# Optimization experiments

Hardware: AMD Instinct MI355X
Metric: run time of the kernel (lower is better)

The kernel has to match this reference:

```python
import jax, jax.numpy as jnp
import numpy as np

N_NODES = 50000
N_GRAPHS = 512
HIDDEN = 128
BN_EPS = 1e-5


def setup_inputs() -> dict:
    key = jax.random.key(0)
    ks = jax.random.split(key, 16)
    E = 800000
    x = jax.random.normal(ks[0], (N_NODES, 1), dtype=jnp.float32)
    pos = jax.random.normal(ks[1], (N_NODES, 3), dtype=jnp.float32)
    edge_index = jax.random.randint(ks[2], (2, E), 0, N_NODES, dtype=jnp.int64)
    batch = jnp.sort(jax.random.randint(ks[3], (N_NODES,), 0, N_GRAPHS, dtype=jnp.int64))

    def lin(k, fan_in, fan_out):
        bound = 1.0 / np.sqrt(fan_in)
        return jax.random.uniform(k, (fan_in, fan_out), jnp.float32, -bound, bound)

    # conv1: in=1 -> concat dim 2*1+3=5
    c1_w1 = lin(ks[4], 5, HIDDEN); c1_b1 = jnp.zeros((HIDDEN,), jnp.float32)
    c1_w2 = lin(ks[5], HIDDEN, HIDDEN); c1_b2 = jnp.zeros((HIDDEN,), jnp.float32)
    # conv2: in=128 -> concat dim 2*128+3=259
    c2_w1 = lin(ks[6], 2 * HIDDEN + 3, HIDDEN); c2_b1 = jnp.zeros((HIDDEN,), jnp.float32)
    c2_w2 = lin(ks[7], HIDDEN, HIDDEN); c2_b2 = jnp.zeros((HIDDEN,), jnp.float32)
    # predictor MLP [128, 128, 1], bias=[False, True], batch_norm + relu between
    p_w1 = lin(ks[8], HIDDEN, HIDDEN)
    bn_gamma = jnp.ones((HIDDEN,), jnp.float32)
    bn_beta = jnp.zeros((HIDDEN,), jnp.float32)
    p_w2 = lin(ks[9], HIDDEN, 1)
    p_b2 = jnp.zeros((1,), jnp.float32)
    return {
        "x": x, "pos": pos, "edge_index": edge_index, "batch": batch,
        "c1_w1": c1_w1, "c1_b1": c1_b1, "c1_w2": c1_w2, "c1_b2": c1_b2,
        "c2_w1": c2_w1, "c2_b1": c2_b1, "c2_w2": c2_w2, "c2_b2": c2_b2,
        "p_w1": p_w1, "bn_gamma": bn_gamma, "bn_beta": bn_beta,
        "p_w2": p_w2, "p_b2": p_b2,
    }


def _conv(x, pos, src, dst, w1, b1, w2, b2):
    # gather endpoints; PyG: x_j = x[src], x_i = x[dst], aggregate into dst
    feat = jnp.concatenate([x[dst], x[src], pos[src] - pos[dst]], axis=-1)  # [E, 2F+3]
    msg = jax.nn.relu(feat @ w1 + b1) @ w2 + b2  # [E, H]
    return jax.ops.segment_sum(msg, dst, num_segments=N_NODES)  # [N, H]


def reference(x, pos, edge_index, batch,
              c1_w1, c1_b1, c1_w2, c1_b2,
              c2_w1, c2_b1, c2_w2, c2_b2,
              p_w1, bn_gamma, bn_beta, p_w2, p_b2):
    src, dst = edge_index[0], edge_index[1]
    h = jax.nn.relu(_conv(x, pos, src, dst, c1_w1, c1_b1, c1_w2, c1_b2))
    h = jax.nn.relu(_conv(h, pos, src, dst, c2_w1, c2_b1, c2_w2, c2_b2))
    g = jax.ops.segment_sum(h, batch, num_segments=N_GRAPHS)  # [G, H] global add pool
    # predictor: Linear(no bias) -> BatchNorm(train stats) -> ReLU -> Linear(bias)
    z = g @ p_w1
    mean = jnp.mean(z, axis=0)
    var = jnp.var(z, axis=0)
    z = bn_gamma * (z - mean) * jax.lax.rsqrt(var + BN_EPS) + bn_beta
    z = jax.nn.relu(z)
    return z @ p_w2 + p_b2  # [G, 1]
```

## Files before the change

### kernel.cpp

```cpp
#include <hip/hip_runtime.h>
#include <hip/hip_bf16.h>

#define HID 128
#define DMAX 64
#define ESHARD 2048

typedef unsigned int uint;
typedef unsigned short ushort;
using short8 = __attribute__((ext_vector_type(8))) short;
using f32x4  = __attribute__((ext_vector_type(4))) float;

#define MFMA_B16(a, b, c) __builtin_amdgcn_mfma_f32_16x16x32_bf16(a, b, c, 0, 0, 0)

__device__ inline ushort bf16rn(float f) {
  uint u = __float_as_uint(f);
  u += 0x7fff + ((u >> 16) & 1);
  return (ushort)(u >> 16);
}
__device__ inline uint packbf(float a, float b) {
  return (uint)bf16rn(a) | ((uint)bf16rn(b) << 16);
}
__device__ inline float bflo(uint u) { return __uint_as_float(u << 16); }
__device__ inline float bfhi(uint u) { return __uint_as_float(u & 0xffff0000u); }

__global__ __launch_bounds__(256) void k_prep(
    const float* __restrict__ x, const float* __restrict__ pos,
    const float* __restrict__ c1w2, const float* __restrict__ c2w1, const float* __restrict__ c2w2,
    float4* __restrict__ xp, int* __restrict__ deg, float* __restrict__ g,
    float* __restrict__ mv,
    ushort* __restrict__ w1t, ushort* __restrict__ wdt,
    ushort* __restrict__ wst, ushort* __restrict__ w2t,
    int N, int G, int Npad) {
  int idx = blockIdx.x * 256 + threadIdx.x;
  if (idx < Npad) deg[idx] = 0;
  if (idx < G * HID) g[idx] = 0.f;
  if (idx < 256) mv[idx] = 0.f;
  if (idx < N) {
    xp[idx] = make_float4(pos[3 * idx], pos[3 * idx + 1], pos[3 * idx + 2], x[idx]);
  }
  {
    int m = idx >> 14, e = idx & 16383;
    int c = e >> 7, k = e & 127;
    const float* src;
    ushort* dst;
    if (m == 0)      { src = c1w2;              dst = w1t; }
    else if (m == 1) { src = c2w1;              dst = wdt; }
    else if (m == 2) { src = c2w1 + 128 * 128;  dst = wst; }
    else             { src = c2w2;              dst = w2t; }
    dst[e] = bf16rn(src[k * 128 + c]);
  }
}

__global__ __launch_bounds__(256) void k_build(const int* __restrict__ dstv,
                                               const int* __restrict__ srcv,
                                               int* __restrict__ deg, int* __restrict__ srcsP,
                                               int E) {
  int shard = blockIdx.x & 7;
  int base = (blockIdx.x >> 3) * ESHARD;
  int lim = min(base + ESHARD, E);
  for (int e = base + threadIdx.x; e < lim; e += 256) {
    int d = dstv[e];
    if (((d >> 5) & 7) == shard) {
      int s = srcv[e];
      int r = atomicAdd(&deg[d], 1);
      if (r < DMAX) srcsP[(size_t)d * DMAX + r] = s;
    }
  }
}

__global__ __launch_bounds__(64) void k_conv1(
    const float4* __restrict__ xp,
    const int* __restrict__ deg, const int* __restrict__ srcsP,
    const float* __restrict__ w1, const float* __restrict__ b1, uint* __restrict__ hs) {
  int n = blockIdx.x;
  int lane = threadIdx.x;
  int f0 = 2 * lane;
  __shared__ float sxs[64];
  __shared__ float sdp[3][64];
  int cnt = min(deg[n], DMAX);
  float4 me = xp[n];
  float xi = me.w;
  float2 a1 = *(const float2*)&w1[HID + f0];
  float2 a2 = *(const float2*)&w1[2 * HID + f0];
  float2 a3 = *(const float2*)&w1[3 * HID + f0];
  float2 a4 = *(const float2*)&w1[4 * HID + f0];
  float c_0 = fmaf(xi, w1[f0],     b1[f0]);
  float c_1 = fmaf(xi, w1[f0 + 1], b1[f0 + 1]);
  float acc0 = 0.f, acc1 = 0.f;
  if (lane < cnt) {
    int s = srcsP[(size_t)n * DMAX + lane];
    float4 v = xp[s];
    sxs[lane] = v.w;
    sdp[0][lane] = v.x - me.x;
    sdp[1][lane] = v.y - me.y;
    sdp[2][lane] = v.z - me.z;
  }
  __syncthreads();
  for (int k = 0; k < cnt; ++k) {
    float xj = sxs[k], d0 = sdp[0][k], d1 = sdp[1][k], d2 = sdp[2][k];
    float h0 = fmaf(xj, a1.x, fmaf(d0, a2.x, fmaf(d1, a3.x, fmaf(d2, a4.x, c_0))));
    float h1 = fmaf(xj, a1.y, fmaf(d0, a2.y, fmaf(d1, a3.y, fmaf(d2, a4.y, c_1))));
    acc0 += fmaxf(h0, 0.f);
    acc1 += fmaxf(h1, 0.f);
  }
  hs[(size_t)n * 64 + lane] = packbf(acc0, acc1);
}

__global__ __launch_bounds__(512) void k_mfuse(
    const ushort* __restrict__ A, const ushort* __restrict__ W1t,
    const ushort* __restrict__ Wdt, const ushort* __restrict__ Wst,
    const float* __restrict__ b1, const float* __restrict__ bd,
    const int* __restrict__ deg,
    uint* __restrict__ psb, uint* __restrict__ pdb, int M) {
  __shared__ uint hl[128][68];
  __shared__ uint hd[128][68];
  int t = threadIdx.x;
  int l = t & 63;
  int rl = l & 15, kg = l >> 4;
  int wv = t >> 6;
  int rs = wv >> 2;
  int ct = wv & 3;
  int rowbase = blockIdx.x * 128 + rs * 64;
  short8 af[4][4];
  float dgv[4];
  #pragma unroll
  for (int rg = 0; rg < 4; ++rg) {
    int r = rowbase + rg * 16 + rl;
    int rc = min(r, M - 1);
    const short8* arow = (const short8*)(A + (size_t)rc * 128);
    #pragma unroll
    for (int k = 0; k < 4; ++k) af[rg][k] = arow[4 * k + kg];
    dgv[rg] = (r < M) ? (float)deg[r] : 0.f;
  }
  #pragma unroll
  for (int j = 0; j < 2; ++j) {
    int nt = ct * 2 + j;
    const short8* wrow = (const short8*)(W1t + (size_t)(nt * 16 + rl) * 128);
    short8 wf[4];
    #pragma unroll
    for (int k = 0; k < 4; ++k) wf[k] = wrow[4 * k + kg];
    int c0 = nt * 16 + kg * 4;
    f32x4 b4 = *(const f32x4*)&b1[c0];
    #pragma unroll
    for (int rg = 0; rg < 4; ++rg) {
      f32x4 acc = {0.f, 0.f, 0.f, 0.f};
      acc = MFMA_B16(wf[0], af[rg][0], acc);
      acc = MFMA_B16(wf[1], af[rg][1], acc);
      acc = MFMA_B16(wf[2], af[rg][2], acc);
      acc = MFMA_B16(wf[3], af[rg][3], acc);
      int rloc = rs * 64 + rg * 16 + rl;
      float v0 = fmaxf(fmaf(dgv[rg], b4[0], acc[0]), 0.f);
      float v1 = fmaxf(fmaf(dgv[rg], b4[1], acc[1]), 0.f);
      float v2 = fmaxf(fmaf(dgv[rg], b4[2], acc[2]), 0.f);
      float v3 = fmaxf(fmaf(dgv[rg], b4[3], acc[3]), 0.f);
      hl[rloc][(c0 >> 1)]     = packbf(v0, v1);
      hl[rloc][(c0 >> 1) + 1] = packbf(v2, v3);
    }
  }
  __syncthreads();
  #pragma unroll
  for (int rg = 0; rg < 4; ++rg) {
    const uint* hrow = hl[rs * 64 + rg * 16 + rl];
    #pragma unroll
    for (int k = 0; k < 4; ++k) af[rg][k] = *(const short8*)&hrow[k * 16 + kg * 4];
  }
  __syncthreads();
  bool isD = (ct >> 1) != 0;
  int ntb = (ct & 1) * 4;
  const ushort* Wm = isD ? Wdt : Wst;
  #pragma unroll
  for (int jj = 0; jj < 4; ++jj) {
    int nt = ntb + jj;
    const short8* wrow = (const short8*)(Wm + (size_t)(nt * 16 + rl) * 128);
    short8 wf[4];
    #pragma unroll
    for (int k = 0; k < 4; ++k) wf[k] = wrow[4 * k + kg];
    int c0 = nt * 16 + kg * 4;
    f32x4 b4 = {0.f, 0.f, 0.f, 0.f};
    if (isD) b4 = *(const f32x4*)&bd[c0];
    #pragma unroll
    for (int rg = 0; rg < 4; ++rg) {
      f32x4 acc = {0.f, 0.f, 0.f, 0.f};
      acc = MFMA_B16(wf[0], af[rg][0], acc);
      acc = MFMA_B16(wf[1], af[rg][1], acc);
      acc = MFMA_B16(wf[2], af[rg][2], acc);
      acc = MFMA_B16(wf[3], af[rg][3], acc);
      int rloc = rs * 64 + rg * 16 + rl;
      uint lo = packbf(acc[0] + b4[0], acc[1] + b4[1]);
      uint hi = packbf(acc[2] + b4[2], acc[3] + b4[3]);
      if (isD) {
        hd[rloc][(c0 >> 1)]     = lo;
        hd[rloc][(c0 >> 1) + 1] = hi;
      } else {
        hl[rloc][(c0 >> 1)]     = lo;
        hl[rloc][(c0 >> 1) + 1] = hi;
      }
    }
  }
  __syncthreads();
  int rb2 = blockIdx.x * 128;
  #pragma unroll
  for (int idx = t; idx < 128 * 16; idx += 512) {
    int row = idx >> 4, c4 = (idx & 15) * 4;
    int gr = rb2 + row;
    if (gr < M) {
      *(uint4*)&psb[(size_t)gr * 64 + c4] = *(const uint4*)&hl[row][c4];
      *(uint4*)&pdb[(size_t)gr * 64 + c4] = *(const uint4*)&hd[row][c4];
    }
  }
}

__global__ __launch_bounds__(64) void k_conv2(
    const float4* __restrict__ xp,
    const int* __restrict__ deg, const int* __restrict__ srcsP,
    const uint* __restrict__ pdb, const uint* __restrict__ ps,
    const float* __restrict__ wc, uint* __restrict__ hs) {
  int n = blockIdx.x;
  int lane = threadIdx.x;
  int eg = lane >> 4;
  int fb = lane & 15;
  int f0 = 8 * fb;
  __shared__ int ssrc[64];
  __shared__ float sdp[3][64];
  int cnt = min(deg[n], DMAX);
  float4 me = xp[n];
  float c0[8], c1[8], c2[8], pdv[8], acc[8];
  uint4 pdu = *(const uint4*)&pdb[(size_t)n * 64 + fb * 4];
  uint pdua[4] = {pdu.x, pdu.y, pdu.z, pdu.w};
  #pragma unroll
  for (int i = 0; i < 4; ++i) {
    pdv[2 * i]     = bflo(pdua[i]);
    pdv[2 * i + 1] = bfhi(pdua[i]);
  }
  #pragma unroll
  for (int i = 0; i < 8; ++i) {
    c0[i]  = wc[f0 + i];
    c1[i]  = wc[HID + f0 + i];
    c2[i]  = wc[2 * HID + f0 + i];
    acc[i] = 0.f;
  }
  if (lane < cnt) {
    int s = srcsP[(size_t)n * DMAX + lane];
    float4 v = xp[s];
    ssrc[lane] = s;
    sdp[0][lane] = v.x - me.x;
    sdp[1][lane] = v.y - me.y;
    sdp[2][lane] = v.z - me.z;
  }
  __syncthreads();
  for (int k = 0; k < cnt; k += 16) {
    int ke[4] = {k + eg, k + 4 + eg, k + 8 + eg, k + 12 + eg};
    int kc[4];
    #pragma unroll
    for (int j = 0; j < 4; ++j) kc[j] = min(ke[j], cnt - 1);
    int se[4] = {ssrc[kc[0]], ssrc[kc[1]], ssrc[kc[2]], ssrc[kc[3]]};
    uint4 u[4];
    #pragma unroll
    for (int j = 0; j < 4; ++j) u[j] = *(const uint4*)&ps[(size_t)se[j] * 64 + fb * 4];
    #pragma unroll
    for (int j = 0; j < 4; ++j) {
      float dd0 = sdp[0][kc[j]], dd1 = sdp[1][kc[j]], dd2 = sdp[2][kc[j]];
      bool vv = ke[j] < cnt;
      uint uu[4] = {u[j].x, u[j].y, u[j].z, u[j].w};
      if (vv) {
        #pragma unroll
        for (int q = 0; q < 4; ++q) {
          float w0  = pdv[2*q]   + fmaf(dd0, c0[2*q],   fmaf(dd1, c1[2*q],   dd2 * c2[2*q]));
          float w1v = pdv[2*q+1] + fmaf(dd0, c0[2*q+1], fmaf(dd1, c1[2*q+1], dd2 * c2[2*q+1]));
          acc[2*q]   += fmaxf(w0  + bflo(uu[q]), 0.f);
          acc[2*q+1] += fmaxf(w1v + bfhi(uu[q]), 0.f);
        }
      }
    }
  }
  #pragma unroll
  for (int i = 0; i < 8; ++i) {
    acc[i] += __shfl_xor(acc[i], 16);
    acc[i] += __shfl_xor(acc[i], 32);
  }
  if (eg == 0) {
    uint4 o;
    o.x = packbf(acc[0], acc[1]);
    o.y = packbf(acc[2], acc[3]);
    o.z = packbf(acc[4], acc[5]);
    o.w = packbf(acc[6], acc[7]);
    *(uint4*)&hs[(size_t)n * 64 + fb * 4] = o;
  }
}

__global__ __launch_bounds__(256) void k_mpool(
    const ushort* __restrict__ A, const ushort* __restrict__ Wt,
    const float* __restrict__ bias, const int* __restrict__ deg, const int* __restrict__ batch,
    float* __restrict__ Of, int M) {
  int t = threadIdx.x;
  int l = t & 63;
  int rl = l & 15, kg = l >> 4;
  int r = blockIdx.x * 64 + (t >> 6) * 16 + rl;
  int rc = min(r, M - 1);
  bool valid = (r < M);
  const short8* arow = (const short8*)(A + (size_t)rc * 128);
  short8 af0 = arow[kg], af1 = arow[4 + kg], af2 = arow[8 + kg], af3 = arow[12 + kg];
  float dg = valid ? (float)deg[r] : 0.f;
  int bt = batch[rc];
  int gf = __shfl(bt, 0);
  int gl = __shfl(bt, 15);
  #pragma unroll
  for (int nt = 0; nt < 8; ++nt) {
    const short8* wrow = (const short8*)(Wt + (size_t)(nt * 16 + rl) * 128);
    f32x4 acc = {0.f, 0.f, 0.f, 0.f};
    acc = MFMA_B16(wrow[kg],      af0, acc);
    acc = MFMA_B16(wrow[4 + kg],  af1, acc);
    acc = MFMA_B16(wrow[8 + kg],  af2, acc);
    acc = MFMA_B16(wrow[12 + kg], af3, acc);
    int c0 = nt * 16 + kg * 4;
    f32x4 b4 = *(const f32x4*)&bias[c0];
    float v0 = valid ? fmaxf(fmaf(dg, b4[0], acc[0]), 0.f) : 0.f;
    float v1 = valid ? fmaxf(fmaf(dg, b4[1], acc[1]), 0.f) : 0.f;
    float v2 = valid ? fmaxf(fmaf(dg, b4[2], acc[2]), 0.f) : 0.f;
    float v3 = valid ? fmaxf(fmaf(dg, b4[3], acc[3]), 0.f) : 0.f;
    for (int gg = gf; gg <= gl; ++gg) {
      bool mine = (bt == gg);
      float s0 = mine ? v0 : 0.f;
      float s1 = mine ? v1 : 0.f;
      float s2 = mine ? v2 : 0.f;
      float s3 = mine ? v3 : 0.f;
      #pragma unroll
      for (int m = 1; m <= 8; m <<= 1) {
        s0 += __shfl_xor(s0, m);
        s1 += __shfl_xor(s1, m);
        s2 += __shfl_xor(s2, m);
        s3 += __shfl_xor(s3, m);
      }
      if (rl == 0) {
        float* gp = &Of[(size_t)gg * 128 + c0];
        atomicAdd(gp + 0, s0);
        atomicAdd(gp + 1, s1);
        atomicAdd(gp + 2, s2);
        atomicAdd(gp + 3, s3);
      }
    }
  }
}

__global__ __launch_bounds__(256) void k_pgemm(
    const float* __restrict__ A, const float* __restrict__ W, float* __restrict__ O1,
    float* __restrict__ mv, int M) {
  __shared__ float As[128][36];
  int t = threadIdx.x;
  int n0 = blockIdx.x * 32;
  int j = t & 127, m = t >> 7;
  for (int idx = t; idx < 32 * 128; idx += 256) {
    int r = idx >> 7, i = idx & 127;
    int n = n0 + r;
    As[i][r] = (n < M) ? A[(size_t)n * 128 + i] : 0.f;
  }
  __syncthreads();
  float acc[16];
  #pragma unroll
  for (int r = 0; r < 16; ++r) acc[r] = 0.f;
  int rb = m * 16;
  for (int i = 0; i < 128; ++i) {
    float w = W[i * 128 + j];
    const float4* ap = reinterpret_cast<const float4*>(&As[i][rb]);
    #pragma unroll
    for (int q = 0; q < 4; ++q) {
      float4 a = ap[q];
      acc[q * 4 + 0] = fmaf(a.x, w, acc[q * 4 + 0]);
      acc[q * 4 + 1] = fmaf(a.y, w, acc[q * 4 + 1]);
      acc[q * 4 + 2] = fmaf(a.z, w, acc[q * 4 + 2]);
      acc[q * 4 + 3] = fmaf(a.w, w, acc[q * 4 + 3]);
    }
  }
  float S = 0.f, Q = 0.f;
  #pragma unroll
  for (int r = 0; r < 16; ++r) {
    int n = n0 + rb + r;
    if (n < M) {
      O1[(size_t)n * 128 + j] = acc[r];
      S += acc[r];
      Q = fmaf(acc[r], acc[r], Q);
    }
  }
  atomicAdd(&mv[j], S);
  atomicAdd(&mv[128 + j], Q);
}

__global__ __launch_bounds__(256) void k_final(
    const float* __restrict__ z, const float* __restrict__ mv,
    const float* __restrict__ gamma, const float* __restrict__ beta,
    const float* __restrict__ w2, const float* __restrict__ b2,
    float* __restrict__ out, int G) {
  int wid = threadIdx.x >> 6, lane = threadIdx.x & 63;
  int r = blockIdx.x * 4 + wid;
  if (r >= G) return;
  float acc = 0.f;
  float invG = 1.f / (float)G;
  #pragma unroll
  for (int h = 0; h < 2; ++h) {
    int jj = lane + h * 64;
    float mean = mv[jj] * invG;
    float var = mv[128 + jj] * invG - mean * mean;
    float rstd = rsqrtf(var + 1e-5f);
    float v = z[(size_t)r * 128 + jj];
    float zn = fmaf((v - mean) * rstd, gamma[jj], beta[jj]);
    acc = fmaf(fmaxf(zn, 0.f), w2[jj], acc);
  }
  #pragma unroll
  for (int off = 32; off; off >>= 1) acc += __shfl_down(acc, off);
  if (lane == 0) out[r] = acc + b2[0];
}

extern "C" void kernel_launch(void* const* d_in, const int* in_sizes, int n_in,
                              void* d_out, int out_size, void* d_ws, size_t ws_size,
                              hipStream_t stream) {
  const float* x     = (const float*)d_in[0];
  const float* pos   = (const float*)d_in[1];
  const int*   eidx  = (const int*)d_in[2];
  const int*   batch = (const int*)d_in[3];
  const float* c1w1  = (const float*)d_in[4];
  const float* c1b1  = (const float*)d_in[5];
  const float* c1w2  = (const float*)d_in[6];
  const float* c1b2  = (const float*)d_in[7];
  const float* c2w1  = (const float*)d_in[8];
  const float* c2b1  = (const float*)d_in[9];
  const float* c2w2  = (const float*)d_in[10];
  const float* c2b2  = (const float*)d_in[11];
  const float* pw1   = (const float*)d_in[12];
  const float* gamma = (const float*)d_in[13];
  const float* beta  = (const float*)d_in[14];
  const float* pw2   = (const float*)d_in[15];
  const float* pb2   = (const float*)d_in[16];
  (void)n_in; (void)ws_size;

  const int N = in_sizes[0];
  const int E = in_sizes[2] / 2;
  const int G = out_size;
  const int* srcv = eidx;
  const int* dstv = eidx + E;

  char* w = (char*)d_ws;
  size_t o = 0;
  auto carve = [&](size_t bytes) { void* p = w + o; o = (o + bytes + 255) & ~(size_t)255; return p; };
  int Npad = ((N + 255) / 256) * 256;
  int* deg    = (int*)carve((size_t)Npad * 4);
  int* srcsP  = (int*)carve((size_t)N * DMAX * 4);
  float4* xp  = (float4*)carve((size_t)N * 16);
  uint*   hs1  = (uint*)carve((size_t)N * 64 * 4);
  uint*   pdb  = (uint*)carve((size_t)N * 64 * 4);
  uint*   psb  = (uint*)carve((size_t)N * 64 * 4);
  uint*   hs2  = (uint*)carve((size_t)N * 64 * 4);
  ushort* w1t  = (ushort*)carve(16384 * 2);
  ushort* wdt  = (ushort*)carve(16384 * 2);
  ushort* wst  = (ushort*)carve(16384 * 2);
  ushort* w2t  = (ushort*)carve(16384 * 2);
  float* g    = (float*)carve((size_t)G * HID * 4);
  float* z    = (float*)carve((size_t)G * HID * 4);
  float* mv   = (float*)carve(256 * 4);

  k_prep<<<256, 256, 0, stream>>>(x, pos, c1w2, c2w1, c2w2,
                                  xp, deg, g, mv, w1t, wdt, wst, w2t, N, G, Npad);
  int nwin = (E + ESHARD - 1) / ESHARD;
  k_build<<<nwin * 8, 256, 0, stream>>>(dstv, srcv, deg, srcsP, E);

  k_conv1<<<N, 64, 0, stream>>>(xp, deg, srcsP, c1w1, c1b1, hs1);
  int gb128 = (N + 127) / 128;
  k_mfuse<<<gb128, 512, 0, stream>>>((const ushort*)hs1, w1t, wdt, wst, c1b2, c2b1, deg,
                                     psb, pdb, N);
  k_conv2<<<N, 64, 0, stream>>>(xp, deg, srcsP, pdb, psb, c2w1 + 256 * HID, hs2);
  int gb = (N + 63) / 64;
  k_mpool<<<gb, 256, 0, stream>>>((const ushort*)hs2, w2t, c2b2, deg, batch, g, N);
  k_pgemm<<<(G + 31) / 32, 256, 0, stream>>>(g, pw1, z, mv, G);
  k_final<<<(G + 3) / 4, 256, 0, stream>>>(z, mv, gamma, beta, pw2, pb2, (float*)d_out, G);
}
```

Baseline: 166.8 us.

## Retile pooled-MLP kernel so each wave covers 64 rows and 32 columns

```diff
diff --git a/kernel.cpp b/kernel.cpp
--- a/kernel.cpp
+++ b/kernel.cpp
@@ -288,55 +288,75 @@
   }
 }
 
-__global__ __launch_bounds__(256) void k_mpool(
+__global__ __launch_bounds__(512) void k_mpool(
     const ushort* __restrict__ A, const ushort* __restrict__ Wt,
     const float* __restrict__ bias, const int* __restrict__ deg, const int* __restrict__ batch,
     float* __restrict__ Of, int M) {
   int t = threadIdx.x;
   int l = t & 63;
   int rl = l & 15, kg = l >> 4;
-  int r = blockIdx.x * 64 + (t >> 6) * 16 + rl;
-  int rc = min(r, M - 1);
-  bool valid = (r < M);
-  const short8* arow = (const short8*)(A + (size_t)rc * 128);
-  short8 af0 = arow[kg], af1 = arow[4 + kg], af2 = arow[8 + kg], af3 = arow[12 + kg];
-  float dg = valid ? (float)deg[r] : 0.f;
-  int bt = batch[rc];
-  int gf = __shfl(bt, 0);
-  int gl = __shfl(bt, 15);
-  #pragma unroll
-  for (int nt = 0; nt < 8; ++nt) {
+  int wv = t >> 6;
+  int rs = wv >> 2;
+  int ct = wv & 3;
+  int rowbase = blockIdx.x * 128 + rs * 64;
+  short8 af[4][4];
+  float dgv[4];
+  int btv[4], gfv[4], glv[4];
+  bool valv[4];
+  #pragma unroll
+  for (int rg = 0; rg < 4; ++rg) {
+    int r = rowbase + rg * 16 + rl;
+    int rc = min(r, M - 1);
+    const short8* arow = (const short8*)(A + (size_t)rc * 128);
+    #pragma unroll
+    for (int k = 0; k < 4; ++k) af[rg][k] = arow[4 * k + kg];
+    valv[rg] = (r < M);
+    dgv[rg] = valv[rg] ? (float)deg[r] : 0.f;
+    int bt = batch[rc];
+    btv[rg] = bt;
+    gfv[rg] = __shfl(bt, 0);
+    glv[rg] = __shfl(bt, 15);
+  }
+  #pragma unroll
+  for (int j = 0; j < 2; ++j) {
+    int nt = ct * 2 + j;
     const short8* wrow = (const short8*)(Wt + (size_t)(nt * 16 + rl) * 128);
-    f32x4 acc = {0.f, 0.f, 0.f, 0.f};
-    acc = MFMA_B16(wrow[kg],      af0, acc);
-    acc = MFMA_B16(wrow[4 + kg],  af1, acc);
-    acc = MFMA_B16(wrow[8 + kg],  af2, acc);
-    acc = MFMA_B16(wrow[12 + kg], af3, acc);
+    short8 wf[4];
+    #pragma unroll
+    for (int k = 0; k < 4; ++k) wf[k] = wrow[4 * k + kg];
     int c0 = nt * 16 + kg * 4;
     f32x4 b4 = *(const f32x4*)&bias[c0];
-    float v0 = valid ? fmaxf(fmaf(dg, b4[0], acc[0]), 0.f) : 0.f;
-    float v1 = valid ? fmaxf(fmaf(dg, b4[1], acc[1]), 0.f) : 0.f;
-    float v2 = valid ? fmaxf(fmaf(dg, b4[2], acc[2]), 0.f) : 0.f;
-    float v3 = valid ? fmaxf(fmaf(dg, b4[3], acc[3]), 0.f) : 0.f;
-    for (int gg = gf; gg <= gl; ++gg) {
-      bool mine = (bt == gg);
-      float s0 = mine ? v0 : 0.f;
-      float s1 = mine ? v1 : 0.f;
-      float s2 = mine ? v2 : 0.f;
-      float s3 = mine ? v3 : 0.f;
-      #pragma unroll
-      for (int m = 1; m <= 8; m <<= 1) {
-        s0 += __shfl_xor(s0, m);
-        s1 += __shfl_xor(s1, m);
-        s2 += __shfl_xor(s2, m);
-        s3 += __shfl_xor(s3, m);
-      }
-      if (rl == 0) {
-        float* gp = &Of[(size_t)gg * 128 + c0];
-        atomicAdd(gp + 0, s0);
-        atomicAdd(gp + 1, s1);
-        atomicAdd(gp + 2, s2);
-        atomicAdd(gp + 3, s3);
+    #pragma unroll
+    for (int rg = 0; rg < 4; ++rg) {
+      f32x4 acc = {0.f, 0.f, 0.f, 0.f};
+      acc = MFMA_B16(wf[0], af[rg][0], acc);
+      acc = MFMA_B16(wf[1], af[rg][1], acc);
+      acc = MFMA_B16(wf[2], af[rg][2], acc);
+      acc = MFMA_B16(wf[3], af[rg][3], acc);
+      float v0 = valv[rg] ? fmaxf(fmaf(dgv[rg], b4[0], acc[0]), 0.f) : 0.f;
+      float v1 = valv[rg] ? fmaxf(fmaf(dgv[rg], b4[1], acc[1]), 0.f) : 0.f;
+      float v2 = valv[rg] ? fmaxf(fmaf(dgv[rg], b4[2], acc[2]), 0.f) : 0.f;
+      float v3 = valv[rg] ? fmaxf(fmaf(dgv[rg], b4[3], acc[3]), 0.f) : 0.f;
+      for (int gg = gfv[rg]; gg <= glv[rg]; ++gg) {
+        bool mine = (btv[rg] == gg);
+        float s0 = mine ? v0 : 0.f;
+        float s1 = mine ? v1 : 0.f;
+        float s2 = mine ? v2 : 0.f;
+        float s3 = mine ? v3 : 0.f;
+        #pragma unroll
+        for (int m = 1; m <= 8; m <<= 1) {
+          s0 += __shfl_xor(s0, m);
+          s1 += __shfl_xor(s1, m);
+          s2 += __shfl_xor(s2, m);
+          s3 += __shfl_xor(s3, m);
+        }
+        if (rl == 0) {
+          float* gp = &Of[(size_t)gg * 128 + c0];
+          atomicAdd(gp + 0, s0);
+          atomicAdd(gp + 1, s1);
+          atomicAdd(gp + 2, s2);
+          atomicAdd(gp + 3, s3);
+        }
       }
     }
   }
@@ -467,8 +487,7 @@
   k_mfuse<<<gb128, 512, 0, stream>>>((const ushort*)hs1, w1t, wdt, wst, c1b2, c2b1, deg,
                                      psb, pdb, N);
   k_conv2<<<N, 64, 0, stream>>>(xp, deg, srcsP, pdb, psb, c2w1 + 256 * HID, hs2);
-  int gb = (N + 63) / 64;
-  k_mpool<<<gb, 256, 0, stream>>>((const ushort*)hs2, w2t, c2b2, deg, batch, g, N);
+  k_mpool<<<gb128, 512, 0, stream>>>((const ushort*)hs2, w2t, c2b2, deg, batch, g, N);
   k_pgemm<<<(G + 31) / 32, 256, 0, stream>>>(g, pw1, z, mv, G);
   k_final<<<(G + 3) / 4, 256, 0, stream>>>(z, mv, gamma, beta, pw2, pb2, (float*)d_out, G);
 }
```

Measured after the change: 168.8 us. Within noise of the previous version (+1.2%).
